# Kernel tuning notes

Hardware: AMD Instinct MI355X
Metric: run time of the kernel (lower is better)

## Reference

```python
import jax, jax.numpy as jnp
import numpy as np

K = 20  # knn neighbors (module default)


def _edge_conv(h, W, s, b):
    # h: [P, C] point features; W: [O, 2C] 1x1 conv weight; s,b: folded BN scale/shift [O]
    g = h @ h.T                                   # [P, P] inner products
    sq = jnp.sum(h * h, axis=-1)                  # [P]
    pd = 2.0 * g - sq[:, None] - sq[None, :]      # negative squared distance (torch knn)
    idx = jax.lax.top_k(pd, K)[1]                 # [P, K] nearest (includes self)
    nb = h[idx]                                   # [P, K, C]
    ctr = jnp.broadcast_to(h[:, None, :], nb.shape)
    edge = jnp.concatenate([nb - ctr, ctr], axis=-1)   # [P, K, 2C]
    y = jnp.einsum('pkc,oc->pko', edge, W)        # 1x1 conv
    y = jax.nn.leaky_relu(y * s + b, 0.2)         # BN (eval, folded) + LeakyReLU
    return jnp.max(y, axis=1)                     # max over neighbors -> [P, O]


def setup_inputs() -> dict:
    key = jax.random.key(0)
    ks = list(jax.random.split(key, 40))
    N, C, B, P = 50000, 128, 16, 1024
    d = {}
    d['features'] = jax.random.normal(ks[0], (N, C), jnp.float32)
    d['clusters'] = jax.random.randint(ks[1], (B, P), 0, N)
    i = 2
    def mk_w(shape):
        nonlocal i
        w = jax.random.normal(ks[i], shape, jnp.float32) * 0.05; i += 1
        return w
    def mk_bn(c):
        nonlocal i
        s = jax.random.uniform(ks[i], (c,), jnp.float32, 0.5, 1.5); i += 1
        b = jax.random.normal(ks[i], (c,), jnp.float32) * 0.1; i += 1
        return s, b
    # EdgeConv blocks: (out, in=2*prev)
    d['W1'] = mk_w((64, 256));  d['s1'], d['b1'] = mk_bn(64)
    d['W2'] = mk_w((64, 128));  d['s2'], d['b2'] = mk_bn(64)
    d['W3'] = mk_w((128, 128)); d['s3'], d['b3'] = mk_bn(128)
    d['W4'] = mk_w((256, 256)); d['s4'], d['b4'] = mk_bn(256)
    d['W5'] = mk_w((512, 512)); d['s5'], d['b5'] = mk_bn(512)
    d['L1'] = mk_w((512, 1024)); d['s6'], d['b6'] = mk_bn(512)
    d['L2'] = mk_w((256, 512)); d['bl2'] = jax.random.normal(ks[i], (256,), jnp.float32) * 0.05; i += 1
    d['s7'], d['b7'] = mk_bn(256)
    d['L3'] = mk_w((1, 256));   d['bl3'] = jax.random.normal(ks[i], (1,), jnp.float32) * 0.05; i += 1
    return d


def reference(clusters, features, W1, s1, b1, W2, s2, b2, W3, s3, b3,
              W4, s4, b4, W5, s5, b5, L1, s6, b6, L2, bl2, s7, b7, L3, bl3):
    def _cluster(h):  # h: [P, 128]
        x1 = _edge_conv(h,  W1, s1, b1)   # [P, 64]
        x2 = _edge_conv(x1, W2, s2, b2)   # [P, 64]
        x3 = _edge_conv(x2, W3, s3, b3)   # [P, 128]
        x4 = _edge_conv(x3, W4, s4, b4)   # [P, 256]
        xc = jnp.concatenate([x1, x2, x3, x4], axis=-1)            # [P, 512]
        y = jax.nn.leaky_relu((xc @ W5.T) * s5 + b5, 0.2)          # conv5 + BN + lrelu
        return jnp.concatenate([jnp.max(y, 0), jnp.mean(y, 0)])    # [1024] max+avg pool

    feat = jax.vmap(_cluster)(features[clusters])                  # [B, 1024]
    z = jax.nn.leaky_relu((feat @ L1.T) * s6 + b6, 0.2)            # dropout = identity (eval)
    z = jax.nn.leaky_relu((z @ L2.T + bl2) * s7 + b7, 0.2)
    z = z @ L3.T + bl3
    return jax.nn.sigmoid(z)                                       # [B, 1]
```

## Files before the change

kernel.cpp:

```cpp
#include <hip/hip_runtime.h>
#include <math.h>

#define KNN 20
#define PPTS 1024
#define NCL 16

typedef _Float16 f16x8 __attribute__((ext_vector_type(8)));
typedef _Float16 f16x4 __attribute__((ext_vector_type(4)));
typedef float f32x4 __attribute__((ext_vector_type(4)));

__device__ __forceinline__ float lrelu(float x) { return x > 0.f ? x : 0.2f * x; }

#define DPPMAX(x, ctrl) { \
    unsigned _t = (unsigned)__builtin_amdgcn_update_dpp((int)(x), (int)(x), ctrl, 0xF, 0xF, false); \
    (x) = (x) > _t ? (x) : _t; }




__global__ void gather_kernel(const float4* __restrict__ feat,
                              const int* __restrict__ clusters,
                              f16x4* __restrict__ hf,
                              float* __restrict__ sqp) {
    int n = blockIdx.x * 256 + threadIdx.x;
    int c4 = n & 31;
    int row = n >> 5;
    int src = clusters[row];
    float4 v = feat[(size_t)src * 32 + c4];
    f16x4 o;
    o[0] = (_Float16)v.x; o[1] = (_Float16)v.y; o[2] = (_Float16)v.z; o[3] = (_Float16)v.w;
    hf[(size_t)(row >> 4) * 512 + (c4 >> 3) * 128 + (row & 15) * 8 + (c4 & 7)] = o;
    float s = v.x * v.x + v.y * v.y + v.z * v.z + v.w * v.w;
    #pragma unroll
    for (int off = 16; off; off >>= 1) s += __shfl_xor(s, off);
    if (c4 == 0) { sqp[2 * row] = s; sqp[2 * row + 1] = 0.f; }
}

__global__ void prep_kernel(const float* __restrict__ W5, f16x4* __restrict__ dst5,
                            const float* __restrict__ W1, f16x4* __restrict__ wn1, f16x4* __restrict__ wv1,
                            const float* __restrict__ W2, f16x4* __restrict__ wn2, f16x4* __restrict__ wv2,
                            const float* __restrict__ W3, f16x4* __restrict__ wn3, f16x4* __restrict__ wv3,
                            const float* __restrict__ W4, f16x4* __restrict__ wn4, f16x4* __restrict__ wv4) {
    int bk = blockIdx.x;
    if (bk < 256) {
        int n = bk * 256 + threadIdx.x;
        int c4 = n & 127;
        int row = n >> 7;
        float4 v = *(const float4*)&W5[(size_t)row * 512 + c4 * 4];
        f16x4 o;
        o[0] = (_Float16)v.x; o[1] = (_Float16)v.y; o[2] = (_Float16)v.z; o[3] = (_Float16)v.w;
        dst5[(size_t)(row >> 4) * 2048 + (c4 >> 3) * 128 + (row & 15) * 8 + (c4 & 7)] = o;
        return;
    }
    const float* W; f16x4* wn; f16x4* wv; int lgC4, n0;
    if (bk < 264)      { W = W1; wn = wn1; wv = wv1; lgC4 = 5; n0 = bk - 256; }
    else if (bk < 268) { W = W2; wn = wn2; wv = wv2; lgC4 = 4; n0 = bk - 264; }
    else if (bk < 276) { W = W3; wn = wn3; wv = wv3; lgC4 = 4; n0 = bk - 268; }
    else               { W = W4; wn = wn4; wv = wv4; lgC4 = 5; n0 = bk - 276; }
    int n = n0 * 256 + threadIdx.x;
    int c4 = n & ((1 << lgC4) - 1);
    int o = n >> lgC4;
    int C = 4 << lgC4;
    float4 a = *(const float4*)&W[(size_t)o * 2 * C + c4 * 4];
    float4 b = *(const float4*)&W[(size_t)o * 2 * C + C + c4 * 4];
    f16x4 on, ov;
    on[0] = (_Float16)a.x; on[1] = (_Float16)a.y; on[2] = (_Float16)a.z; on[3] = (_Float16)a.w;
    ov[0] = (_Float16)(b.x - a.x); ov[1] = (_Float16)(b.y - a.y);
    ov[2] = (_Float16)(b.z - a.z); ov[3] = (_Float16)(b.w - a.w);
    size_t ti = (size_t)(o >> 4) * (C * 4) + (c4 >> 3) * 128 + (o & 15) * 8 + (c4 & 7);
    wn[ti] = on; wv[ti] = ov;
}

template<int C>
__global__ __launch_bounds__(1024, 8) void grampk_kernel(
    const _Float16* __restrict__ hf,
    const float* __restrict__ sqp, int* __restrict__ idx)
{
    __shared__ unsigned keys[16 * 1024];
    const int f = blockIdx.x;
    const int g = f >> 3;
    const int b = (f & 7) + 8 * (g >> 6);
    const int bxi = g & 63;
    const _Float16* hb = hf + (size_t)b * PPTS * C;
    const float* sqb = sqp + 2 * (b << 10);
    const int w = threadIdx.x >> 6;
    const int lane = threadIdx.x & 63;
    const int col16 = lane & 15, quad = lane >> 4;
    const int i0 = bxi * 16;
    const int j0 = w * 64;
    const _Float16* aB = hb + (size_t)bxi * 16 * C + col16 * 32 + quad * 8;
    const _Float16* bB = hb + (size_t)(w * 4) * 16 * C + col16 * 32 + quad * 8;
    f32x4 acc[4] = {};
    #pragma unroll
    for (int kc = 0; kc < C / 32; kc++) {
        f16x8 a = *(const f16x8*)&aB[kc * 512];
        #pragma unroll
        for (int t = 0; t < 4; t++) {
            f16x8 bf = *(const f16x8*)&bB[(size_t)t * 16 * C + kc * 512];
            acc[t] = __builtin_amdgcn_mfma_f32_16x16x32_f16(a, bf, acc[t], 0, 0, 0);
        }
    }
    #pragma unroll
    for (int t = 0; t < 4; t++) {
        int j = j0 + t * 16 + col16;
        float sqj = sqb[2 * j] + sqb[2 * j + 1];
        #pragma unroll
        for (int r = 0; r < 4; r++) {
            int row = quad * 4 + r;
            float val = __builtin_fmaf(2.f, acc[t][r], -sqj);
            unsigned u = __float_as_uint(val);
            unsigned key = (u & 0x80000000u) ? ~u : (u | 0x80000000u);
            keys[(row << 10) | ((j + 2 * row) & 1023)] = (key & 0xFFFFFC00u) | (unsigned)j;
        }
    }
    __syncthreads();
    {
        const int row = w;
        const unsigned* krow = &keys[row << 10];
        unsigned m1 = 0u, m2 = 0u, m3 = 0u;
        #pragma unroll
        for (int s = 0; s < 16; s++) {
            unsigned x = krow[s * 64 + lane];
            unsigned h1 = x > m1 ? x : m1, l1 = x < m1 ? x : m1;
            unsigned h2 = l1 > m2 ? l1 : m2, l2 = l1 < m2 ? l1 : m2;
            unsigned h3 = l2 > m3 ? l2 : m3;
            m1 = h1; m2 = h2; m3 = h3;
        }
        unsigned myout = 0;
        for (int kk = 0; kk < KNN; kk++) {
            unsigned x = m1;
            DPPMAX(x, 0xB1);
            DPPMAX(x, 0x4E);
            DPPMAX(x, 0x141);
            DPPMAX(x, 0x140);
            DPPMAX(x, 0x142);
            DPPMAX(x, 0x143);
            unsigned gm = (unsigned)__builtin_amdgcn_readlane((int)x, 63);
            if (lane == kk) myout = gm & 1023u;
            if (m1 == gm) {
                if (m2 != 0u) {
                    m1 = m2; m2 = m3; m3 = 0u;
                } else {
                    unsigned n1 = 0u, n2 = 0u, n3 = 0u;
                    #pragma unroll
                    for (int s = 0; s < 16; s++) {
                        unsigned x2 = krow[s * 64 + lane];
                        x2 = x2 < gm ? x2 : 0u;
                        unsigned h1 = x2 > n1 ? x2 : n1, l1 = x2 < n1 ? x2 : n1;
                        unsigned h2 = l1 > n2 ? l1 : n2, l2 = l1 < n2 ? l1 : n2;
                        unsigned h3 = l2 > n3 ? l2 : n3;
                        n1 = h1; n2 = h2; n3 = h3;
                    }
                    m1 = n1; m2 = n2; m3 = n3;
                }
            }
        }
        if (lane < KNN) idx[((size_t)b * PPTS + i0 + row) * KNN + lane] = (int)myout;
    }
}

template<int C>
__global__ __launch_bounds__(256, 4) void uv_mfma_kernel(
    const _Float16* __restrict__ hf, int lgO,
    const _Float16* __restrict__ wn, const _Float16* __restrict__ wv,
    float* __restrict__ U, float* __restrict__ V)
{
    constexpr int NBLK = 4 * (C / 32);
    __shared__ _Float16 nsh[NBLK * 640];
    __shared__ _Float16 vsh[NBLK * 640];
    const int O = 1 << lgO;
    const int f = blockIdx.x;
    const int r = f >> 3;
    const int c = (f & 7) + 8 * (r >> (lgO - 2));
    const int i2 = r & ((1 << (lgO - 2)) - 1);
    const int ox = i2 & ((O >> 6) - 1);
    const int yy = i2 >> (lgO - 6);
    const int w = threadIdx.x >> 6;
    const int lane = threadIdx.x & 63;
    const int col16 = lane & 15, quad = lane >> 4;
    const int r0 = (c * 16 + yy) * 64 + w * 16;
    const int o0 = ox * 64;
    const _Float16* aB = hf + (size_t)(r0 >> 4) * 16 * C + col16 * 32 + quad * 8;
    const _Float16* nS = wn + (size_t)(o0 >> 4) * 16 * C;
    const _Float16* vS = wv + (size_t)(o0 >> 4) * 16 * C;

    #pragma unroll
    for (int p = 0; p < C / 32; p++) {
        int h = (p * 256 + (int)threadIdx.x) * 8;
        int blk = h >> 9, col = (h >> 5) & 15, q = (h >> 3) & 3;
        int d = blk * 640 + col * 40 + q * 8;
        *(f16x8*)&nsh[d] = *(const f16x8*)&nS[h];
        *(f16x8*)&vsh[d] = *(const f16x8*)&vS[h];
    }
    __syncthreads();

    f32x4 au[4] = {}, av[4] = {};
    #pragma unroll
    for (int kc = 0; kc < C / 32; kc++) {
        f16x8 a = *(const f16x8*)&aB[kc * 512];
        #pragma unroll
        for (int t = 0; t < 4; t++) {
            int d = (t * (C / 32) + kc) * 640 + col16 * 40 + quad * 8;
            f16x8 bn = *(const f16x8*)&nsh[d];
            au[t] = __builtin_amdgcn_mfma_f32_16x16x32_f16(a, bn, au[t], 0, 0, 0);
            f16x8 bv = *(const f16x8*)&vsh[d];
            av[t] = __builtin_amdgcn_mfma_f32_16x16x32_f16(a, bv, av[t], 0, 0, 0);
        }
    }
    #pragma unroll
    for (int t = 0; t < 4; t++) {
        int o = o0 + t * 16 + col16;
        #pragma unroll
        for (int r2 = 0; r2 < 4; r2++) {
            int p = r0 + quad * 4 + r2;
            U[((size_t)p << lgO) + o] = au[t][r2];
            V[((size_t)p << lgO) + o] = av[t][r2];
        }
    }
}

__global__ void agg_kernel(const float* __restrict__ U, const float* __restrict__ V,
                           const int* __restrict__ idx, int lgO,
                           const float* __restrict__ sc, const float* __restrict__ bi,
                           _Float16* __restrict__ hnext,
                           _Float16* __restrict__ xcf, int co,
                           float* __restrict__ sqp)
{
    int O = 1 << lgO;
    int f = blockIdx.x;
    int rr = f >> 3;
    int c = (f & 7) + 8 * (rr >> (lgO + 2));
    int ii = rr & ((1 << (lgO + 2)) - 1);
    int n = (((c << (lgO + 2)) + ii) << 8) + threadIdx.x;
    int o = n & (O - 1);
    int pr = n >> lgO;
    int b = pr >> 10;
    const int* id = idx + (size_t)pr * KNN;
    float m = -INFINITY;
    #pragma unroll
    for (int k = 0; k < KNN; k++) {
        int j = id[k];
        float u = U[((size_t)(b * PPTS + j) << lgO) + o];
        m = fmaxf(m, u);
    }
    float val = lrelu((m + V[((size_t)pr << lgO) + o]) * sc[o] + bi[o]);
    _Float16 hv = (_Float16)val;
    int prg = pr >> 4, prr = pr & 15;
    xcf[(size_t)prg * 8192 + ((co + o) >> 5) * 512 + prr * 32 + (o & 31)] = hv;
    if (hnext) {
        hnext[(size_t)prg * 16 * O + (o >> 5) * 512 + prr * 32 + (o & 31)] = hv;
        float s = val * val;
        #pragma unroll
        for (int off = 32; off; off >>= 1) s += __shfl_xor(s, off);
        if ((threadIdx.x & 63) == 0) {
            sqp[2 * pr + ((o >> 6) & 1)] = s;
            if (lgO == 6) sqp[2 * pr + 1] = 0.f;
        }
    }
}

__global__ __launch_bounds__(256, 4) void conv5pool_kernel(
    const _Float16* __restrict__ xcf, const _Float16* __restrict__ w5f,
    const float* __restrict__ s5, const float* __restrict__ b5,
    float* __restrict__ pmax, float* __restrict__ psum)
{
    __shared__ _Float16 bsh[2][8 * 640];
    __shared__ float lmax[4][128], lsum[4][128];
    const int f = blockIdx.x;
    const int r = f >> 3;
    const int c = (f & 7) + 8 * (r >> 5);
    const int within = r & 31;
    const int pb = within >> 2;
    const int ob = within & 3;
    const int w = threadIdx.x >> 6;
    const int lane = threadIdx.x & 63;
    const int col16 = lane & 15, quad = lane >> 4;
    const int p0 = (c * 8 + pb) * 128 + w * 32;
    const int o0 = ob * 128;
    const _Float16* aB = xcf + (size_t)(p0 >> 4) * 8192 + col16 * 32 + quad * 8;
    const _Float16* bS = w5f + (size_t)(o0 >> 4) * 8192;

    auto stage = [&](int kc, int buf) {
        #pragma unroll
        for (int s = 0; s < 2; s++) {
            int h = (s * 256 + (int)threadIdx.x) * 8;
            int t = h >> 9, rr2 = (h >> 5) & 15, q = (h >> 3) & 3;
            f16x8 x = *(const f16x8*)&bS[(size_t)t * 8192 + kc * 512 + rr2 * 32 + q * 8];
            *(f16x8*)&bsh[buf][t * 640 + rr2 * 40 + q * 8] = x;
        }
    };

    stage(0, 0);
    f32x4 acc[2][8] = {};
    for (int kc = 0; kc < 16; kc++) {
        int cur = kc & 1;
        __syncthreads();
        if (kc < 15) stage(kc + 1, cur ^ 1);
        f16x8 a0 = *(const f16x8*)&aB[kc * 512];
        f16x8 a1 = *(const f16x8*)&aB[8192 + kc * 512];
        #pragma unroll
        for (int t = 0; t < 8; t++) {
            f16x8 bf = *(const f16x8*)&bsh[cur][t * 640 + col16 * 40 + quad * 8];
            acc[0][t] = __builtin_amdgcn_mfma_f32_16x16x32_f16(a0, bf, acc[0][t], 0, 0, 0);
            acc[1][t] = __builtin_amdgcn_mfma_f32_16x16x32_f16(a1, bf, acc[1][t], 0, 0, 0);
        }
    }
    #pragma unroll
    for (int t = 0; t < 8; t++) {
        int o = o0 + t * 16 + col16;
        float sc = s5[o], bi = b5[o];
        float vm = -INFINITY, vs = 0.f;
        #pragma unroll
        for (int u = 0; u < 2; u++)
            #pragma unroll
            for (int r2 = 0; r2 < 4; r2++) {
                float val = lrelu(acc[u][t][r2] * sc + bi);
                vm = fmaxf(vm, val); vs += val;
            }
        #pragma unroll
        for (int off = 16; off < 64; off <<= 1) {
            vm = fmaxf(vm, __shfl_xor(vm, off));
            vs += __shfl_xor(vs, off);
        }
        if (quad == 0) { lmax[w][t * 16 + col16] = vm; lsum[w][t * 16 + col16] = vs; }
    }
    __syncthreads();
    if (threadIdx.x < 128) {
        int col = threadIdx.x;
        float m = lmax[0][col], s = lsum[0][col];
        #pragma unroll
        for (int q = 1; q < 4; q++) { m = fmaxf(m, lmax[q][col]); s += lsum[q][col]; }
        size_t o = (size_t)(c * 8 + pb) * 512 + o0 + col;
        pmax[o] = m; psum[o] = s;
    }
}

__global__ void poolred_kernel(const float* __restrict__ pmax, const float* __restrict__ psum,
                               float* __restrict__ feat) {
    int n = blockIdx.x * 256 + threadIdx.x;
    int o = n & 511, cl = n >> 9;
    float m = -INFINITY, s = 0.f;
    #pragma unroll
    for (int c = 0; c < 8; c++) {
        size_t q = (size_t)(cl * 8 + c) * 512 + o;
        m = fmaxf(m, pmax[q]); s += psum[q];
    }
    feat[(size_t)cl * 1024 + o] = m;
    feat[(size_t)cl * 1024 + 512 + o] = s * (1.f / 1024.f);
}

__global__ void mlp1_kernel(const float* __restrict__ feat, const float* __restrict__ L1,
                            const float* __restrict__ s6, const float* __restrict__ b6,
                            float* __restrict__ z1) {
    int wid = (blockIdx.x * 256 + threadIdx.x) >> 6;
    int lane = threadIdx.x & 63;
    int o = wid & 511, b = wid >> 9;
    const float* f = feat + (size_t)b * 1024;
    const float* w = L1 + (size_t)o * 1024;
    float acc = 0.f;
    #pragma unroll
    for (int i = 0; i < 16; i++) acc = fmaf(f[i * 64 + lane], w[i * 64 + lane], acc);
    #pragma unroll
    for (int off = 32; off; off >>= 1) acc += __shfl_xor(acc, off);
    if (lane == 0) z1[wid] = lrelu(acc * s6[o] + b6[o]);
}

__global__ void mlp2_kernel(const float* __restrict__ z1, const float* __restrict__ L2,
                            const float* __restrict__ bl2,
                            const float* __restrict__ s7, const float* __restrict__ b7,
                            float* __restrict__ z2) {
    int wid = (blockIdx.x * 256 + threadIdx.x) >> 6;
    int lane = threadIdx.x & 63;
    int o = wid & 255, b = wid >> 8;
    const float* f = z1 + (size_t)b * 512;
    const float* w = L2 + (size_t)o * 512;
    float acc = 0.f;
    #pragma unroll
    for (int i = 0; i < 8; i++) acc = fmaf(f[i * 64 + lane], w[i * 64 + lane], acc);
    #pragma unroll
    for (int off = 32; off; off >>= 1) acc += __shfl_xor(acc, off);
    if (lane == 0) z2[wid] = lrelu((acc + bl2[o]) * s7[o] + b7[o]);
}

__global__ void mlp3_kernel(const float* __restrict__ z2, const float* __restrict__ L3,
                            const float* __restrict__ bl3, float* __restrict__ out) {
    __shared__ float red[256];
    int t = threadIdx.x;
    int b = t >> 4, q = t & 15;
    float acc = 0.f;
    for (int c = q * 16; c < q * 16 + 16; c++) acc = fmaf(z2[(size_t)b * 256 + c], L3[c], acc);
    red[t] = acc;
    __syncthreads();
    if (q == 0) {
        float s = 0.f;
        #pragma unroll
        for (int i = 0; i < 16; i++) s += red[b * 16 + i];
        s += bl3[0];
        out[b] = 1.f / (1.f + expf(-s));
    }
}

extern "C" void kernel_launch(void* const* d_in, const int* in_sizes, int n_in,
                              void* d_out, int out_size, void* d_ws, size_t ws_size,
                              hipStream_t stream) {
    const float* features = (const float*)d_in[0];
    const int*   clusters = (const int*)d_in[1];
    const float* W1 = (const float*)d_in[2];
    const float* s1 = (const float*)d_in[3];
    const float* b1 = (const float*)d_in[4];
    const float* W2 = (const float*)d_in[5];
    const float* s2 = (const float*)d_in[6];
    const float* b2 = (const float*)d_in[7];
    const float* W3 = (const float*)d_in[8];
    const float* s3 = (const float*)d_in[9];
    const float* b3 = (const float*)d_in[10];
    const float* W4 = (const float*)d_in[11];
    const float* s4 = (const float*)d_in[12];
    const float* b4 = (const float*)d_in[13];
    const float* W5 = (const float*)d_in[14];
    const float* s5 = (const float*)d_in[15];
    const float* b5 = (const float*)d_in[16];
    const float* L1 = (const float*)d_in[17];
    const float* s6 = (const float*)d_in[18];
    const float* b6 = (const float*)d_in[19];
    const float* L2 = (const float*)d_in[20];
    const float* bl2 = (const float*)d_in[21];
    const float* s7 = (const float*)d_in[22];
    const float* b7 = (const float*)d_in[23];
    const float* L3 = (const float*)d_in[24];
    const float* bl3 = (const float*)d_in[25];

    float* ws = (float*)d_ws;
    float* U   = ws;
    float* V   = U + 4194304;
    _Float16* xcf16 = (_Float16*)(V + 4194304);
    _Float16* w5f16 = xcf16 + 8388608;
    _Float16* hf16  = w5f16 + 262144;
    _Float16* wnA   = hf16 + 2097152;
    _Float16* wvA   = wnA + 131072;
    int*   idx  = (int*)(wvA + 131072);
    float* sqp  = (float*)(idx + 327680);
    float* pmax = sqp + 32768;
    float* psum = pmax + 131072;
    float* feat = psum + 131072;
    float* z1   = feat + 16384;
    float* z2   = z1 + 8192;

    _Float16* wn[4] = { wnA, wnA + 32768, wnA + 65536, wnA + 98304 };
    _Float16* wv[4] = { wvA, wvA + 32768, wvA + 65536, wvA + 98304 };

    gather_kernel<<<2048, 256, 0, stream>>>((const float4*)features, clusters,
                                            (f16x4*)hf16, sqp);
    prep_kernel<<<308, 256, 0, stream>>>(W5, (f16x4*)w5f16,
                                         W1, (f16x4*)wn[0], (f16x4*)wv[0],
                                         W2, (f16x4*)wn[1], (f16x4*)wv[1],
                                         W3, (f16x4*)wn[2], (f16x4*)wv[2],
                                         W4, (f16x4*)wn[3], (f16x4*)wv[3]);

    auto stage = [&](int si, int C, int O, int lgO,
                     const float* sc, const float* bi,
                     int co, _Float16* hnext) {
        if (C == 128)
            grampk_kernel<128><<<1024, 1024, 0, stream>>>(hf16, sqp, idx);
        else
            grampk_kernel<64><<<1024, 1024, 0, stream>>>(hf16, sqp, idx);
        if (C == 128)
            uv_mfma_kernel<128><<<(O >> 6) * 256, 256, 0, stream>>>(hf16, lgO, wn[si], wv[si], U, V);
        else
            uv_mfma_kernel<64><<<(O >> 6) * 256, 256, 0, stream>>>(hf16, lgO, wn[si], wv[si], U, V);
        agg_kernel<<<(NCL * PPTS * O) / 256, 256, 0, stream>>>(U, V, idx, lgO, sc, bi,
                                                               hnext, xcf16, co, sqp);
    };

    stage(0, 128,  64, 6, s1, b1, 0,   hf16);
    stage(1,  64,  64, 6, s2, b2, 64,  hf16);
    stage(2,  64, 128, 7, s3, b3, 128, hf16);
    stage(3, 128, 256, 8, s4, b4, 256, (_Float16*)nullptr);

    conv5pool_kernel<<<512, 256, 0, stream>>>(xcf16, w5f16, s5, b5, pmax, psum);
    poolred_kernel<<<32, 256, 0, stream>>>(pmax, psum, feat);
    mlp1_kernel<<<2048, 256, 0, stream>>>(feat, L1, s6, b6, z1);
    mlp2_kernel<<<1024, 256, 0, stream>>>(z1, L2, bl2, s7, b7, z2);
    mlp3_kernel<<<1, 256, 0, stream>>>(z2, L3, bl3, (float*)d_out);
}
```

Baseline: 341.0 us.

## Merge kNN gram/top-k and U/V projection into one heterogeneous launch

Combines the grampk and uv_mfma kernels into a single stagefu kernel. Blocks below NU compute the U/V projections, with four of the former 256-thread sub-blocks packed into each 1024-thread block. The remaining blocks do the gram matrix plus top-k selection. This removes one launch per stage and lets the two independent workloads run at the same time. In exchange, shared memory is a 64KB union, launch bounds drop to 4 blocks per CU, and the U/V blocks now occupy 1024 threads each.

```diff
diff --git a/kernel.cpp b/kernel.cpp
--- a/kernel.cpp
+++ b/kernel.cpp
@@ -72,149 +72,145 @@
 }
 
 template<int C>
-__global__ __launch_bounds__(1024, 8) void grampk_kernel(
-    const _Float16* __restrict__ hf,
-    const float* __restrict__ sqp, int* __restrict__ idx)
+__global__ __launch_bounds__(1024, 4) void stagefu_kernel(
+    const _Float16* __restrict__ hf, const float* __restrict__ sqp,
+    int* __restrict__ idx, int lgO, int NU,
+    const _Float16* __restrict__ wn, const _Float16* __restrict__ wv,
+    float* __restrict__ U, float* __restrict__ V)
 {
-    __shared__ unsigned keys[16 * 1024];
-    const int f = blockIdx.x;
-    const int g = f >> 3;
-    const int b = (f & 7) + 8 * (g >> 6);
-    const int bxi = g & 63;
-    const _Float16* hb = hf + (size_t)b * PPTS * C;
-    const float* sqb = sqp + 2 * (b << 10);
+    __shared__ char smem[65536];
     const int w = threadIdx.x >> 6;
     const int lane = threadIdx.x & 63;
     const int col16 = lane & 15, quad = lane >> 4;
-    const int i0 = bxi * 16;
-    const int j0 = w * 64;
-    const _Float16* aB = hb + (size_t)bxi * 16 * C + col16 * 32 + quad * 8;
-    const _Float16* bB = hb + (size_t)(w * 4) * 16 * C + col16 * 32 + quad * 8;
-    f32x4 acc[4] = {};
-    #pragma unroll
-    for (int kc = 0; kc < C / 32; kc++) {
-        f16x8 a = *(const f16x8*)&aB[kc * 512];
+
+    if ((int)blockIdx.x < NU) {
+        _Float16* nsh = (_Float16*)smem;
+        _Float16* vsh = nsh + (4 * (C / 32)) * 640;
+        const int O = 1 << lgO;
+        const int k = blockIdx.x;
+        const int s = w >> 2;
+        const int wsub = w & 3;
+        const int fp = k * 4 + s;
+        const int r = fp >> 3;
+        const int c = (fp & 7) + 8 * (r >> (lgO - 2));
+        const int i2 = r & ((1 << (lgO - 2)) - 1);
+        const int ox = i2 & ((O >> 6) - 1);
+        const int yy = i2 >> (lgO - 6);
+        const int r0 = (c * 16 + yy) * 64 + wsub * 16;
+        const int o0 = ox * 64;
+        const _Float16* aB = hf + (size_t)(r0 >> 4) * 16 * C + col16 * 32 + quad * 8;
+        const _Float16* nS = wn + (size_t)(o0 >> 4) * 16 * C;
+        const _Float16* vS = wv + (size_t)(o0 >> 4) * 16 * C;
+        int tid = threadIdx.x;
+        if (tid * 8 < 64 * C) {
+            int h = tid * 8;
+            int blk = h >> 9, col = (h >> 5) & 15, q = (h >> 3) & 3;
+            int d = blk * 640 + col * 40 + q * 8;
+            *(f16x8*)&nsh[d] = *(const f16x8*)&nS[h];
+            *(f16x8*)&vsh[d] = *(const f16x8*)&vS[h];
+        }
+        __syncthreads();
+        f32x4 au[4] = {}, av[4] = {};
+        #pragma unroll
+        for (int kc = 0; kc < C / 32; kc++) {
+            f16x8 a = *(const f16x8*)&aB[kc * 512];
+            #pragma unroll
+            for (int t = 0; t < 4; t++) {
+                int d = (t * (C / 32) + kc) * 640 + col16 * 40 + quad * 8;
+                f16x8 bn = *(const f16x8*)&nsh[d];
+                au[t] = __builtin_amdgcn_mfma_f32_16x16x32_f16(a, bn, au[t], 0, 0, 0);
+                f16x8 bv = *(const f16x8*)&vsh[d];
+                av[t] = __builtin_amdgcn_mfma_f32_16x16x32_f16(a, bv, av[t], 0, 0, 0);
+            }
+        }
         #pragma unroll
         for (int t = 0; t < 4; t++) {
-            f16x8 bf = *(const f16x8*)&bB[(size_t)t * 16 * C + kc * 512];
-            acc[t] = __builtin_amdgcn_mfma_f32_16x16x32_f16(a, bf, acc[t], 0, 0, 0);
-        }
-    }
-    #pragma unroll
-    for (int t = 0; t < 4; t++) {
-        int j = j0 + t * 16 + col16;
-        float sqj = sqb[2 * j] + sqb[2 * j + 1];
-        #pragma unroll
-        for (int r = 0; r < 4; r++) {
-            int row = quad * 4 + r;
-            float val = __builtin_fmaf(2.f, acc[t][r], -sqj);
-            unsigned u = __float_as_uint(val);
-            unsigned key = (u & 0x80000000u) ? ~u : (u | 0x80000000u);
-            keys[(row << 10) | ((j + 2 * row) & 1023)] = (key & 0xFFFFFC00u) | (unsigned)j;
-        }
-    }
-    __syncthreads();
-    {
-        const int row = w;
-        const unsigned* krow = &keys[row << 10];
-        unsigned m1 = 0u, m2 = 0u, m3 = 0u;
-        #pragma unroll
-        for (int s = 0; s < 16; s++) {
-            unsigned x = krow[s * 64 + lane];
-            unsigned h1 = x > m1 ? x : m1, l1 = x < m1 ? x : m1;
-            unsigned h2 = l1 > m2 ? l1 : m2, l2 = l1 < m2 ? l1 : m2;
-            unsigned h3 = l2 > m3 ? l2 : m3;
-            m1 = h1; m2 = h2; m3 = h3;
-        }
-        unsigned myout = 0;
-        for (int kk = 0; kk < KNN; kk++) {
-            unsigned x = m1;
-            DPPMAX(x, 0xB1);
-            DPPMAX(x, 0x4E);
-            DPPMAX(x, 0x141);
-            DPPMAX(x, 0x140);
-            DPPMAX(x, 0x142);
-            DPPMAX(x, 0x143);
-            unsigned gm = (unsigned)__builtin_amdgcn_readlane((int)x, 63);
-            if (lane == kk) myout = gm & 1023u;
-            if (m1 == gm) {
-                if (m2 != 0u) {
-                    m1 = m2; m2 = m3; m3 = 0u;
-                } else {
-                    unsigned n1 = 0u, n2 = 0u, n3 = 0u;
-                    #pragma unroll
-                    for (int s = 0; s < 16; s++) {
-                        unsigned x2 = krow[s * 64 + lane];
-                        x2 = x2 < gm ? x2 : 0u;
-                        unsigned h1 = x2 > n1 ? x2 : n1, l1 = x2 < n1 ? x2 : n1;
-                        unsigned h2 = l1 > n2 ? l1 : n2, l2 = l1 < n2 ? l1 : n2;
-                        unsigned h3 = l2 > n3 ? l2 : n3;
-                        n1 = h1; n2 = h2; n3 = h3;
+            int o = o0 + t * 16 + col16;
+            #pragma unroll
+            for (int r2 = 0; r2 < 4; r2++) {
+                int p = r0 + quad * 4 + r2;
+                U[((size_t)p << lgO) + o] = au[t][r2];
+                V[((size_t)p << lgO) + o] = av[t][r2];
+            }
+        }
+    } else {
+        unsigned* keys = (unsigned*)smem;
+        const int f = (int)blockIdx.x - NU;
+        const int g = f >> 3;
+        const int b = (f & 7) + 8 * (g >> 6);
+        const int bxi = g & 63;
+        const _Float16* hb = hf + (size_t)b * PPTS * C;
+        const float* sqb = sqp + 2 * (b << 10);
+        const int i0 = bxi * 16;
+        const int j0 = w * 64;
+        const _Float16* aB = hb + (size_t)bxi * 16 * C + col16 * 32 + quad * 8;
+        const _Float16* bB = hb + (size_t)(w * 4) * 16 * C + col16 * 32 + quad * 8;
+        f32x4 acc[4] = {};
+        #pragma unroll
+        for (int kc = 0; kc < C / 32; kc++) {
+            f16x8 a = *(const f16x8*)&aB[kc * 512];
+            #pragma unroll
+            for (int t = 0; t < 4; t++) {
+                f16x8 bf = *(const f16x8*)&bB[(size_t)t * 16 * C + kc * 512];
+                acc[t] = __builtin_amdgcn_mfma_f32_16x16x32_f16(a, bf, acc[t], 0, 0, 0);
+            }
+        }
+        #pragma unroll
+        for (int t = 0; t < 4; t++) {
+            int j = j0 + t * 16 + col16;
+            float sqj = sqb[2 * j] + sqb[2 * j + 1];
+            #pragma unroll
+            for (int r = 0; r < 4; r++) {
+                int row = quad * 4 + r;
+                float val = __builtin_fmaf(2.f, acc[t][r], -sqj);
+                unsigned u = __float_as_uint(val);
+                unsigned key = (u & 0x80000000u) ? ~u : (u | 0x80000000u);
+                keys[(row << 10) | ((j + 2 * row) & 1023)] = (key & 0xFFFFFC00u) | (unsigned)j;
+            }
+        }
+        __syncthreads();
+        {
+            const int row = w;
+            const unsigned* krow = &keys[row << 10];
+            unsigned m1 = 0u, m2 = 0u, m3 = 0u;
+            #pragma unroll
+            for (int s = 0; s < 16; s++) {
+                unsigned x = krow[s * 64 + lane];
+                unsigned h1 = x > m1 ? x : m1, l1 = x < m1 ? x : m1;
+                unsigned h2 = l1 > m2 ? l1 : m2, l2 = l1 < m2 ? l1 : m2;
+                unsigned h3 = l2 > m3 ? l2 : m3;
+                m1 = h1; m2 = h2; m3 = h3;
+            }
+            unsigned myout = 0;
+            for (int kk = 0; kk < KNN; kk++) {
+                unsigned x = m1;
+                DPPMAX(x, 0xB1);
+                DPPMAX(x, 0x4E);
+                DPPMAX(x, 0x141);
+                DPPMAX(x, 0x140);
+                DPPMAX(x, 0x142);
+                DPPMAX(x, 0x143);
+                unsigned gm = (unsigned)__builtin_amdgcn_readlane((int)x, 63);
+                if (lane == kk) myout = gm & 1023u;
+                if (m1 == gm) {
+                    if (m2 != 0u) {
+                        m1 = m2; m2 = m3; m3 = 0u;
+                    } else {
+                        unsigned n1 = 0u, n2 = 0u, n3 = 0u;
+                        #pragma unroll
+                        for (int s = 0; s < 16; s++) {
+                            unsigned x2 = krow[s * 64 + lane];
+                            x2 = x2 < gm ? x2 : 0u;
+                            unsigned h1 = x2 > n1 ? x2 : n1, l1 = x2 < n1 ? x2 : n1;
+                            unsigned h2 = l1 > n2 ? l1 : n2, l2 = l1 < n2 ? l1 : n2;
+                            unsigned h3 = l2 > n3 ? l2 : n3;
+                            n1 = h1; n2 = h2; n3 = h3;
+                        }
+                        m1 = n1; m2 = n2; m3 = n3;
                     }
-                    m1 = n1; m2 = n2; m3 = n3;
                 }
             }
-        }
-        if (lane < KNN) idx[((size_t)b * PPTS + i0 + row) * KNN + lane] = (int)myout;
-    }
-}
-
-template<int C>
-__global__ __launch_bounds__(256, 4) void uv_mfma_kernel(
-    const _Float16* __restrict__ hf, int lgO,
-    const _Float16* __restrict__ wn, const _Float16* __restrict__ wv,
-    float* __restrict__ U, float* __restrict__ V)
-{
-    constexpr int NBLK = 4 * (C / 32);
-    __shared__ _Float16 nsh[NBLK * 640];
-    __shared__ _Float16 vsh[NBLK * 640];
-    const int O = 1 << lgO;
-    const int f = blockIdx.x;
-    const int r = f >> 3;
-    const int c = (f & 7) + 8 * (r >> (lgO - 2));
-    const int i2 = r & ((1 << (lgO - 2)) - 1);
-    const int ox = i2 & ((O >> 6) - 1);
-    const int yy = i2 >> (lgO - 6);
-    const int w = threadIdx.x >> 6;
-    const int lane = threadIdx.x & 63;
-    const int col16 = lane & 15, quad = lane >> 4;
-    const int r0 = (c * 16 + yy) * 64 + w * 16;
-    const int o0 = ox * 64;
-    const _Float16* aB = hf + (size_t)(r0 >> 4) * 16 * C + col16 * 32 + quad * 8;
-    const _Float16* nS = wn + (size_t)(o0 >> 4) * 16 * C;
-    const _Float16* vS = wv + (size_t)(o0 >> 4) * 16 * C;
-
-    #pragma unroll
-    for (int p = 0; p < C / 32; p++) {
-        int h = (p * 256 + (int)threadIdx.x) * 8;
-        int blk = h >> 9, col = (h >> 5) & 15, q = (h >> 3) & 3;
-        int d = blk * 640 + col * 40 + q * 8;
-        *(f16x8*)&nsh[d] = *(const f16x8*)&nS[h];
-        *(f16x8*)&vsh[d] = *(const f16x8*)&vS[h];
-    }
-    __syncthreads();
-
-    f32x4 au[4] = {}, av[4] = {};
-    #pragma unroll
-    for (int kc = 0; kc < C / 32; kc++) {
-        f16x8 a = *(const f16x8*)&aB[kc * 512];
-        #pragma unroll
-        for (int t = 0; t < 4; t++) {
-            int d = (t * (C / 32) + kc) * 640 + col16 * 40 + quad * 8;
-            f16x8 bn = *(const f16x8*)&nsh[d];
-            au[t] = __builtin_amdgcn_mfma_f32_16x16x32_f16(a, bn, au[t], 0, 0, 0);
-            f16x8 bv = *(const f16x8*)&vsh[d];
-            av[t] = __builtin_amdgcn_mfma_f32_16x16x32_f16(a, bv, av[t], 0, 0, 0);
-        }
-    }
-    #pragma unroll
-    for (int t = 0; t < 4; t++) {
-        int o = o0 + t * 16 + col16;
-        #pragma unroll
-        for (int r2 = 0; r2 < 4; r2++) {
-            int p = r0 + quad * 4 + r2;
-            U[((size_t)p << lgO) + o] = au[t][r2];
-            V[((size_t)p << lgO) + o] = av[t][r2];
+            if (lane < KNN) idx[((size_t)b * PPTS + i0 + row) * KNN + lane] = (int)myout;
         }
     }
 }
@@ -460,14 +456,13 @@
     auto stage = [&](int si, int C, int O, int lgO,
                      const float* sc, const float* bi,
                      int co, _Float16* hnext) {
+        int NU = (O >> 6) * 64;
         if (C == 128)
-            grampk_kernel<128><<<1024, 1024, 0, stream>>>(hf16, sqp, idx);
+            stagefu_kernel<128><<<NU + 1024, 1024, 0, stream>>>(hf16, sqp, idx, lgO, NU,
+                                                                wn[si], wv[si], U, V);
         else
-            grampk_kernel<64><<<1024, 1024, 0, stream>>>(hf16, sqp, idx);
-        if (C == 128)
-            uv_mfma_kernel<128><<<(O >> 6) * 256, 256, 0, stream>>>(hf16, lgO, wn[si], wv[si], U, V);
-        else
-            uv_mfma_kernel<64><<<(O >> 6) * 256, 256, 0, stream>>>(hf16, lgO, wn[si], wv[si], U, V);
+            stagefu_kernel<64><<<NU + 1024, 1024, 0, stream>>>(hf16, sqp, idx, lgO, NU,
+                                                               wn[si], wv[si], U, V);
         agg_kernel<<<(NCL * PPTS * O) / 256, 256, 0, stream>>>(U, V, idx, lgO, sc, bi,
                                                                hnext, xcf16, co, sqp);
     };
```

New measurement: 363.3 us. 1.07x slower.
